# Performance work log

Measured on AMD Instinct MI355X. Metric: run time of the kernel, lower is better.

The kernel has to match this reference:

```python
import jax, jax.numpy as jnp
import numpy as np

# ---- dims (match init_kwargs) ----
IMG = 128; PATCH = 16; GRID = IMG // PATCH; L = GRID * GRID  # 64 patches
D = 256            # embed_dim
EXP = 2; DIN = D * EXP          # d_inner = 512
DH = 64; H = DIN // DH          # 8 heads
G = 1; N = 64                   # n_groups, d_state
DCONV = 4
DEPTH = 2
NCLS = 1000
BATCH = 16
DINPROJ = 2 * DIN + 2 * G * N + H   # z | xBC | dt
CDIM = DIN + 2 * G * N              # conv channels
EPS = 1e-6

def _snake_indices():
    g = np.arange(L).reshape(GRID, GRID)
    g[1::2] = g[1::2, ::-1]
    return jnp.asarray(g.reshape(-1))

SNAKE = _snake_indices()

def rmsnorm(x, w):
    return x * jax.lax.rsqrt(jnp.mean(x * x, axis=-1, keepdims=True) + EPS) * w

def causal_depthwise_conv(x, w, b):
    # x: (B,L,C), w: (C,K) depthwise causal conv, then SiLU
    xp = jnp.pad(x, ((0, 0), (DCONV - 1, 0), (0, 0)))
    y = sum(xp[:, k:k + x.shape[1], :] * w[:, k] for k in range(DCONV))
    return jax.nn.silu(y + b)

def mamba_block(x, Win, cw, cb, dtb, Alog, Dp, gn, Wout):
    # Mamba-2/3 style selective scan block. x: (B,L,D)
    Bsz, Lx, _ = x.shape
    zxbcdt = x @ Win                                   # (B,L,DINPROJ)
    z   = zxbcdt[..., :DIN]
    xBC = zxbcdt[..., DIN:DIN + CDIM]
    dt  = jax.nn.softplus(zxbcdt[..., DIN + CDIM:] + dtb)   # (B,L,H)
    xBC = causal_depthwise_conv(xBC, cw, cb)
    xs = xBC[..., :DIN].reshape(Bsz, Lx, H, DH)
    Bm = xBC[..., DIN:DIN + G * N].reshape(Bsz, Lx, G, N)
    Cm = xBC[..., DIN + G * N:].reshape(Bsz, Lx, G, N)
    Bh = jnp.repeat(Bm, H // G, axis=2)                # (B,L,H,N)
    Ch = jnp.repeat(Cm, H // G, axis=2)
    decay = jnp.exp(dt * (-jnp.exp(Alog)))             # (B,L,H) in (0,1)
    dBx = jnp.einsum('blh,blhp,blhn->blhpn', dt, xs, Bh)
    def step(h, inp):
        d, u = inp
        h = d[..., None, None] * h + u
        return h, h
    _, hs = jax.lax.scan(step, jnp.zeros((Bsz, H, DH, N), x.dtype),
                         (jnp.moveaxis(decay, 1, 0), jnp.moveaxis(dBx, 1, 0)))
    hs = jnp.moveaxis(hs, 0, 1)                        # (B,L,H,DH,N)
    y = jnp.einsum('blhpn,blhn->blhp', hs, Ch) + Dp[None, None, :, None] * xs
    y = y.reshape(Bsz, Lx, DIN)
    y = rmsnorm(y * jax.nn.silu(z), gn)                # gated RMSNorm
    return y @ Wout                                    # (B,L,D)

def setup_inputs() -> dict:
    key = jax.random.key(0)
    ks = jax.random.split(key, 24)
    s_in = 1.0 / np.sqrt(D); s_out = 1.0 / np.sqrt(DIN)
    def blk(k):
        kk = jax.random.split(k, 8)
        return dict(
            Win=jax.random.normal(kk[0], (DEPTH, D, DINPROJ)) * s_in,
            cw=jax.random.normal(kk[1], (DEPTH, CDIM, DCONV)) * 0.3,
            cb=jnp.zeros((DEPTH, CDIM)),
            dtb=jax.random.normal(kk[2], (DEPTH, H)) * 0.1,
            Alog=jnp.log(jax.random.uniform(kk[3], (DEPTH, H), minval=1.0, maxval=16.0)),
            Dp=jnp.ones((DEPTH, H)),
            gn=jnp.ones((DEPTH, DIN)),
            Wout=jax.random.normal(kk[4], (DEPTH, DIN, D)) * s_out)
    f = blk(ks[0]); b = blk(ks[1])
    inp = {
        'x': jax.random.normal(ks[2], (BATCH, 3, IMG, IMG), dtype=jnp.float32),
        'patch_w': jax.random.normal(ks[3], (D, 3 * PATCH * PATCH)) * (1.0 / np.sqrt(3 * PATCH * PATCH)),
        'patch_b': jnp.zeros((D,)),
        'pos_embed': jax.random.normal(ks[4], (1, L, D)) * 0.02,
        'norms_w': jnp.ones((DEPTH, D)),
        'final_w': jnp.ones((D,)),
        'head_w': jax.random.normal(ks[5], (D, NCLS)) * (1.0 / np.sqrt(D)),
        'head_b': jnp.zeros((NCLS,)),
    }
    for nm, v in f.items():
        inp[nm + '_f'] = v
    for nm, v in b.items():
        inp[nm + '_b'] = v
    return inp

def reference(x, patch_w, patch_b, pos_embed, norms_w, final_w, head_w, head_b,
              Win_f, cw_f, cb_f, dtb_f, Alog_f, Dp_f, gn_f, Wout_f,
              Win_b, cw_b, cb_b, dtb_b, Alog_b, Dp_b, gn_b, Wout_b):
    Bsz = x.shape[0]
    # patch embed == Conv2d(kernel=stride=PATCH)
    p = x.reshape(Bsz, 3, GRID, PATCH, GRID, PATCH).transpose(0, 2, 4, 1, 3, 5)
    p = p.reshape(Bsz, L, 3 * PATCH * PATCH)
    t = p @ patch_w.T + patch_b                        # (B,L,D)
    t = t + pos_embed[0]
    t = t[:, SNAKE, :]                                 # snake scan order
    for i in range(DEPTH):
        nx = rmsnorm(t, norms_w[i])
        of = mamba_block(nx, Win_f[i], cw_f[i], cb_f[i], dtb_f[i], Alog_f[i], Dp_f[i], gn_f[i], Wout_f[i])
        ob = mamba_block(nx[:, ::-1, :], Win_b[i], cw_b[i], cb_b[i], dtb_b[i], Alog_b[i], Dp_b[i], gn_b[i], Wout_b[i])[:, ::-1, :]
        t = t + 0.5 * (of + ob)                        # drop_path_rate=0 -> identity
    t = rmsnorm(t, final_w)
    t = t.mean(axis=1)
    return t @ head_w + head_b
```

## Files before the change

### kernel.cpp

```cpp
#include <hip/hip_runtime.h>
#include <hip/hip_bf16.h>
#include <math.h>

#define IMG 128
#define PATCH 16
#define L 64
#define D 256
#define DIN 512
#define DH 64
#define H 8
#define NSTATE 64
#define DCONV 4
#define DEPTH 2
#define NCLS 1000
#define BATCH 16
#define DINPROJ 1160
#define CDIM 640
#define EPS 1e-6f

typedef __attribute__((ext_vector_type(8))) short short8;
typedef __attribute__((ext_vector_type(4))) float f32x4;
typedef __attribute__((ext_vector_type(4))) unsigned short us4;
typedef unsigned short ushort_t;

__device__ __forceinline__ int snake_tok(int s){
    int r = s >> 3, c = s & 7;
    return (r & 1) ? (r * 8 + (7 - c)) : (r * 8 + c);
}
__device__ __forceinline__ float silu_f(float x){ return x / (1.f + expf(-x)); }
__device__ __forceinline__ float softplus_f(float x){ return x > 20.f ? x : log1pf(expf(x)); }
__device__ __forceinline__ ushort_t f2b(float f){
    __hip_bfloat16 h = __float2bfloat16(f);
    return *(ushort_t*)&h;
}

__device__ __forceinline__ float block_sum256(float v){
    __shared__ float sm[4];
    #pragma unroll
    for (int o = 32; o > 0; o >>= 1) v += __shfl_down(v, o);
    if ((threadIdx.x & 63) == 0) sm[threadIdx.x >> 6] = v;
    __syncthreads();
    return sm[0] + sm[1] + sm[2] + sm[3];
}

__global__ __launch_bounds__(256) void wconv_patch_k(
    const float* __restrict__ Win0, const float* __restrict__ Win1,
    const float* __restrict__ Wout0, const float* __restrict__ Wout1,
    ushort_t* __restrict__ wbuf,
    const float* __restrict__ x, const float* __restrict__ PW,
    float* __restrict__ part)
{
    __shared__ float sm[32][33];
    __shared__ __align__(16) ushort_t As[2][64][40];
    __shared__ __align__(16) ushort_t Bs[2][64][40];
    const int zall = blockIdx.z;
    if (zall < 8){
        int z = zall;
        int R, C; const float* src; ushort_t* dst;
        if (z < 4){
            int layer = z >> 1, dir = z & 1;
            src = (dir ? Win1 : Win0) + (size_t)layer * D * DINPROJ;
            dst = wbuf + (size_t)z * 296960;
            R = D; C = DINPROJ;
        } else {
            int zz = z - 4, layer = zz >> 1, dir = zz & 1;
            src = (dir ? Wout1 : Wout0) + (size_t)layer * DIN * D;
            dst = wbuf + 1187840 + (size_t)zz * 131072;
            R = DIN; C = D;
        }
        int ctiles = (C + 31) >> 5, rtiles = R >> 5;
        if (blockIdx.x >= ctiles || blockIdx.y >= rtiles) return;
        int c0 = blockIdx.x * 32, r0 = blockIdx.y * 32;
        int tx = threadIdx.x & 31, ty = threadIdx.x >> 5;
        #pragma unroll
        for (int k = 0; k < 4; ++k){
            int r = r0 + ty + 8 * k, c = c0 + tx;
            sm[ty + 8 * k][tx] = (c < C) ? src[(size_t)r * C + c] : 0.f;
        }
        __syncthreads();
        #pragma unroll
        for (int k = 0; k < 4; ++k){
            int dr = c0 + ty + 8 * k, dc = r0 + tx;
            if (dr < C) dst[(size_t)dr * R + dc] = f2b(sm[tx][ty + 8 * k]);
        }
        return;
    }
    if (blockIdx.x >= 4) return;
    const int t = threadIdx.x;
    const int n0 = blockIdx.x * 64;
    const int b  = blockIdx.y;
    const int split = zall - 8;
    const int kbase = split * 96;
    const int lrow = t >> 2, lc8 = (t & 3) * 8;
    const int tok = snake_tok(lrow), gy = tok >> 3, gx = tok & 7;
    const float* xb = x + (size_t)b * 3 * IMG * IMG;
    const int wave = t >> 6, lane = t & 63;
    const int wm = (wave >> 1) * 32, wn = (wave & 1) * 32;
    const int fro = lane & 15, fk = (lane >> 4) * 8;

    f32x4 acc[2][2];
    #pragma unroll
    for (int i = 0; i < 2; ++i)
        #pragma unroll
        for (int j = 0; j < 2; ++j) acc[i][j] = (f32x4){0.f,0.f,0.f,0.f};

    short8 areg, breg;
    auto gload = [&](int kk){
        int k = kk + lc8;
        int c = k >> 8, rem = k & 255, py = rem >> 4, px = rem & 15;
        const float* srcA = xb + ((size_t)c * IMG + gy * PATCH + py) * IMG + gx * PATCH + px;
        float4 a0 = *(const float4*)(srcA);
        float4 a1 = *(const float4*)(srcA + 4);
        ushort_t ta[8] = {f2b(a0.x),f2b(a0.y),f2b(a0.z),f2b(a0.w),
                          f2b(a1.x),f2b(a1.y),f2b(a1.z),f2b(a1.w)};
        areg = *(short8*)ta;
        const float* srcB = PW + (size_t)(n0 + lrow) * 768 + kk + lc8;
        float4 b0 = *(const float4*)(srcB);
        float4 b1 = *(const float4*)(srcB + 4);
        ushort_t tb[8] = {f2b(b0.x),f2b(b0.y),f2b(b0.z),f2b(b0.w),
                          f2b(b1.x),f2b(b1.y),f2b(b1.z),f2b(b1.w)};
        breg = *(short8*)tb;
    };
    auto sstore = [&](int buf){
        *(short8*)&As[buf][lrow][lc8] = areg;
        *(short8*)&Bs[buf][lrow][lc8] = breg;
    };

    const int nk = 3;
    gload(kbase); sstore(0);
    __syncthreads();
    for (int kt = 0; kt < nk; ++kt){
        const int buf = kt & 1;
        if (kt + 1 < nk) gload(kbase + (kt + 1) * 32);
        short8 af[2], bfr[2];
        af[0]  = *(const short8*)&As[buf][wm + fro][fk];
        af[1]  = *(const short8*)&As[buf][wm + 16 + fro][fk];
        bfr[0] = *(const short8*)&Bs[buf][wn + fro][fk];
        bfr[1] = *(const short8*)&Bs[buf][wn + 16 + fro][fk];
        #pragma unroll
        for (int i = 0; i < 2; ++i)
            #pragma unroll
            for (int j = 0; j < 2; ++j)
                acc[i][j] = __builtin_amdgcn_mfma_f32_16x16x32_bf16(af[i], bfr[j], acc[i][j], 0, 0, 0);
        if (kt + 1 < nk) sstore(buf ^ 1);
        __syncthreads();
    }
    float* Cp = part + (size_t)split * (BATCH * L * D);
    #pragma unroll
    for (int i = 0; i < 2; ++i){
        #pragma unroll
        for (int j = 0; j < 2; ++j){
            int col = n0 + wn + j * 16 + (lane & 15);
            #pragma unroll
            for (int r = 0; r < 4; ++r){
                int srow = wm + i * 16 + (lane >> 4) * 4 + r;
                Cp[(size_t)(b * 64 + srow) * D + col] = acc[i][j][r];
            }
        }
    }
}

__global__ void patch_red_k(const float* __restrict__ part, const float* __restrict__ pb,
                            const float* __restrict__ pos, float* __restrict__ t){
    int i = blockIdx.x * 256 + threadIdx.x;
    int d = i & (D - 1), s = (i >> 8) & (L - 1);
    float v = 0.f;
    #pragma unroll
    for (int r = 0; r < 8; ++r) v += part[i + r * (BATCH * L * D)];
    t[i] = v + pb[d] + pos[snake_tok(s) * D + d];
}

__global__ __launch_bounds__(256) void gemm_in_k(
    const float* __restrict__ T, const float* __restrict__ nw,
    const ushort_t* __restrict__ B0, const ushort_t* __restrict__ B1,
    const float* __restrict__ cw0, const float* __restrict__ cw1,
    const float* __restrict__ cb0, const float* __restrict__ cb1,
    const float* __restrict__ dtb0, const float* __restrict__ dtb1,
    const float* __restrict__ Al0, const float* __restrict__ Al1,
    float* __restrict__ zb0, float* __restrict__ zb1,
    float* __restrict__ xy0, float* __restrict__ xy1,
    float* __restrict__ bc0, float* __restrict__ bc1,
    float* __restrict__ dts0, float* __restrict__ dts1,
    float* __restrict__ cums0, float* __restrict__ cums1)
{
    __shared__ __align__(16) ushort_t As[64][264];
    __shared__ __align__(16) ushort_t Bs[2][64][40];
    __shared__ float Ctile[64][68];
    const int dir = blockIdx.z;
    const ushort_t* __restrict__ Bw = dir ? B1 : B0;
    const int t = threadIdx.x;
    const int m0 = blockIdx.y * 64, n0 = blockIdx.x * 64;
    const int b = blockIdx.y;
    const int arow = t >> 2;
    const int wave = t >> 6, lane = t & 63;
    const int wm = (wave >> 1) * 32, wn = (wave & 1) * 32;
    const int fro = lane & 15, fk = (lane >> 4) * 8;

    {
        const float* src = T + (size_t)(m0 + arow) * D;
        float ss = 0.f;
        #pragma unroll
        for (int i = 0; i < 16; ++i){
            int c = (t & 3) * 4 + i * 16;
            float4 v = *(const float4*)(src + c);
            ss += v.x*v.x + v.y*v.y + v.z*v.z + v.w*v.w;
        }
        ss += __shfl_xor(ss, 1);
        ss += __shfl_xor(ss, 2);
        float sc = rsqrtf(ss * (1.f / (float)D) + EPS);
        #pragma unroll
        for (int i = 0; i < 16; ++i){
            int c = (t & 3) * 4 + i * 16;
            float4 v = *(const float4*)(src + c);
            float4 w = *(const float4*)(nw + c);
            us4 o = {f2b(v.x*sc*w.x), f2b(v.y*sc*w.y), f2b(v.z*sc*w.z), f2b(v.w*sc*w.w)};
            *(us4*)&As[arow][c] = o;
        }
    }
    const int lrow = t >> 2, lc8 = (t & 3) * 8;
    float4 breg;
    auto gloadB = [&](int kk){
        int gn = n0 + lrow;
        if (gn < DINPROJ) breg = *(const float4*)(Bw + (size_t)gn * D + kk + lc8);
        else breg = make_float4(0.f,0.f,0.f,0.f);
    };
    auto sstoreB = [&](int buf){ *(float4*)&Bs[buf][lrow][lc8] = breg; };

    f32x4 acc[2][2];
    #pragma unroll
    for (int i = 0; i < 2; ++i)
        #pragma unroll
        for (int j = 0; j < 2; ++j) acc[i][j] = (f32x4){0.f,0.f,0.f,0.f};

    gloadB(0); sstoreB(0);
    __syncthreads();
    const int nk = D / 32;
    for (int kt = 0; kt < nk; ++kt){
        const int buf = kt & 1;
        if (kt + 1 < nk) gloadB((kt + 1) * 32);
        short8 af[2], bfr[2];
        af[0]  = *(const short8*)&As[wm + fro][kt * 32 + fk];
        af[1]  = *(const short8*)&As[wm + 16 + fro][kt * 32 + fk];
        bfr[0] = *(const short8*)&Bs[buf][wn + fro][fk];
        bfr[1] = *(const short8*)&Bs[buf][wn + 16 + fro][fk];
        #pragma unroll
        for (int i = 0; i < 2; ++i)
            #pragma unroll
            for (int j = 0; j < 2; ++j)
                acc[i][j] = __builtin_amdgcn_mfma_f32_16x16x32_bf16(af[i], bfr[j], acc[i][j], 0, 0, 0);
        if (kt + 1 < nk) sstoreB(buf ^ 1);
        __syncthreads();
    }

    if (n0 < DIN){
        float* zb = dir ? zb1 : zb0;
        #pragma unroll
        for (int i = 0; i < 2; ++i){
            #pragma unroll
            for (int j = 0; j < 2; ++j){
                int col = n0 + wn + j * 16 + (lane & 15);
                #pragma unroll
                for (int r = 0; r < 4; ++r){
                    int row = m0 + wm + i * 16 + (lane >> 4) * 4 + r;
                    zb[(size_t)row * DIN + col] = acc[i][j][r];
                }
            }
        }
        return;
    }

    #pragma unroll
    for (int i = 0; i < 2; ++i){
        #pragma unroll
        for (int j = 0; j < 2; ++j){
            int lcol = wn + j * 16 + (lane & 15);
            #pragma unroll
            for (int r = 0; r < 4; ++r){
                int lr = wm + i * 16 + (lane >> 4) * 4 + r;
                Ctile[lr][lcol] = acc[i][j][r];
            }
        }
    }
    __syncthreads();

    if (n0 < 1152){
        const float* cw = dir ? cw1 : cw0;
        const float* cb = dir ? cb1 : cb0;
        float* xy = dir ? xy1 : xy0;
        float* bc = dir ? bc1 : bc0;
        const int c = t & 63;
        const int cc = n0 - DIN + c;
        const float w0 = cw[cc * DCONV + 0], w1 = cw[cc * DCONV + 1];
        const float w2 = cw[cc * DCONV + 2], w3 = cw[cc * DCONV + 3];
        const float bb = cb[cc];
        #pragma unroll
        for (int rep = 0; rep < 16; ++rep){
            int s = (t >> 6) + rep * 4;
            float a = bb;
            {
                int sp = s - 3;
                if (sp >= 0) a += w0 * Ctile[dir ? 63 - sp : sp][c];
                sp = s - 2;
                if (sp >= 0) a += w1 * Ctile[dir ? 63 - sp : sp][c];
                sp = s - 1;
                if (sp >= 0) a += w2 * Ctile[dir ? 63 - sp : sp][c];
                a += w3 * Ctile[dir ? 63 - s : s][c];
            }
            float v = silu_f(a);
            if (cc < DIN) xy[(size_t)(b * 64 + s) * DIN + cc] = v;
            else          bc[(size_t)(b * 64 + s) * 128 + (cc - DIN)] = v;
        }
        return;
    }

    {
        const float* dtb = dir ? dtb1 : dtb0;
        const float* Al  = dir ? Al1  : Al0;
        float* dts  = dir ? dts1  : dts0;
        float* cums = dir ? cums1 : cums0;
        int s = t & 63;
        int l = dir ? (63 - s) : s;
        #pragma unroll
        for (int rep = 0; rep < 2; ++rep){
            int h = (t >> 6) + rep * 4;
            float raw = Ctile[l][h] + dtb[h];
            float dt = softplus_f(raw);
            float val = -expf(Al[h]) * dt;
            #pragma unroll
            for (int o = 1; o < 64; o <<= 1){
                float u = __shfl_up(val, o);
                if (s >= o) val += u;
            }
            dts[(size_t)(b * 64 + s) * H + h]  = dt;
            cums[(size_t)(b * 64 + s) * H + h] = val;
        }
    }
}

__global__ __launch_bounds__(256) void gemm_out_k(
    const ushort_t* __restrict__ A0, const ushort_t* __restrict__ A1,
    const ushort_t* __restrict__ B0, const ushort_t* __restrict__ B1,
    float* __restrict__ part)
{
    __shared__ __align__(16) ushort_t As[2][64][40];
    __shared__ __align__(16) ushort_t Bs[2][64][40];
    const int t = threadIdx.x;
    const int n0 = blockIdx.x * 64, m0 = blockIdx.y * 64;
    const int z = blockIdx.z;
    const int dir = z >> 2;
    const int kbase = (z & 3) * 128;
    const ushort_t* __restrict__ A = dir ? A1 : A0;
    const ushort_t* __restrict__ B = dir ? B1 : B0;
    const int lrow = t >> 2, lc8 = (t & 3) * 8;
    const int wave = t >> 6, lane = t & 63;
    const int wm = (wave >> 1) * 32, wn = (wave & 1) * 32;
    const int fro = lane & 15, fk = (lane >> 4) * 8;

    float4 areg, breg;
    auto gload = [&](int kk){
        areg = *(const float4*)(A + (size_t)(m0 + lrow) * DIN + kk + lc8);
        breg = *(const float4*)(B + (size_t)(n0 + lrow) * DIN + kk + lc8);
    };
    auto sstore = [&](int buf){
        *(float4*)&As[buf][lrow][lc8] = areg;
        *(float4*)&Bs[buf][lrow][lc8] = breg;
    };

    f32x4 acc[2][2];
    #pragma unroll
    for (int i = 0; i < 2; ++i)
        #pragma unroll
        for (int j = 0; j < 2; ++j) acc[i][j] = (f32x4){0.f,0.f,0.f,0.f};

    const int nk = 4;
    gload(kbase); sstore(0);
    __syncthreads();
    for (int kt = 0; kt < nk; ++kt){
        const int buf = kt & 1;
        if (kt + 1 < nk) gload(kbase + (kt + 1) * 32);
        short8 af[2], bfr[2];
        af[0]  = *(const short8*)&As[buf][wm + fro][fk];
        af[1]  = *(const short8*)&As[buf][wm + 16 + fro][fk];
        bfr[0] = *(const short8*)&Bs[buf][wn + fro][fk];
        bfr[1] = *(const short8*)&Bs[buf][wn + 16 + fro][fk];
        #pragma unroll
        for (int i = 0; i < 2; ++i)
            #pragma unroll
            for (int j = 0; j < 2; ++j)
                acc[i][j] = __builtin_amdgcn_mfma_f32_16x16x32_bf16(af[i], bfr[j], acc[i][j], 0, 0, 0);
        if (kt + 1 < nk) sstore(buf ^ 1);
        __syncthreads();
    }
    float* Cp = part + (size_t)z * (BATCH * L * D);
    #pragma unroll
    for (int i = 0; i < 2; ++i){
        #pragma unroll
        for (int j = 0; j < 2; ++j){
            int col = n0 + wn + j * 16 + (lane & 15);
            #pragma unroll
            for (int r = 0; r < 4; ++r){
                int row = m0 + wm + i * 16 + (lane >> 4) * 4 + r;
                Cp[(size_t)row * D + col] = acc[i][j][r];
            }
        }
    }
}

__global__ void out_red_k(const float* __restrict__ part, float* __restrict__ t){
    int i = blockIdx.x * 256 + threadIdx.x;
    float v = 0.f;
    #pragma unroll
    for (int r = 0; r < 8; ++r) v += part[i + r * (BATCH * L * D)];
    t[i] += 0.5f * v;
}

__global__ __launch_bounds__(512) void yscan2_k(
    const float* __restrict__ bc0, const float* __restrict__ bc1,
    const float* __restrict__ dts0, const float* __restrict__ dts1,
    const float* __restrict__ cums0, const float* __restrict__ cums1,
    const float* __restrict__ Dp0, const float* __restrict__ Dp1,
    float* __restrict__ xy0, float* __restrict__ xy1)
{
    __shared__ float Bc[64][65];
    __shared__ float CX[64][65];
    __shared__ float Am[64][65];
    __shared__ float cumS[64], dtS[64];
    const int h = blockIdx.x, b = blockIdx.y, dir = blockIdx.z;
    const float* bc   = dir ? bc1   : bc0;
    const float* dts  = dir ? dts1  : dts0;
    const float* cums = dir ? cums1 : cums0;
    const float* Dp   = dir ? Dp1   : Dp0;
    float* xy = dir ? xy1 : xy0;
    const int t = threadIdx.x;

    if (t < 64){
        cumS[t] = cums[(size_t)(b * L + t) * H + h];
        dtS[t]  = dts[(size_t)(b * L + t) * H + h];
    }
    for (int i = t; i < 4096; i += 512){
        int s = i >> 6, n = i & 63;
        Bc[s][n] = bc[(size_t)(b * L + s) * 128 + n];
        CX[s][n] = bc[(size_t)(b * L + s) * 128 + 64 + n];
    }
    __syncthreads();
    for (int i = t; i < 4096; i += 512){
        int s = i >> 6, j = i & 63;
        float v = 0.f;
        if (j <= s){
            float acc = 0.f;
            #pragma unroll
            for (int n = 0; n < 64; ++n) acc += CX[s][n] * Bc[j][n];
            v = acc * expf(cumS[s] - cumS[j]) * dtS[j];
        }
        Am[s][j] = v;
    }
    __syncthreads();
    for (int i = t; i < 4096; i += 512){
        int j = i >> 6, p = i & 63;
        CX[j][p] = xy[(size_t)(b * L + j) * DIN + h * DH + p];
    }
    __syncthreads();
    float dp = Dp[h];
    for (int i = t; i < 4096; i += 512){
        int s = i >> 6, p = i & 63;
        float acc = dp * CX[s][p];
        #pragma unroll
        for (int j = 0; j < 64; ++j) acc += Am[s][j] * CX[j][p];
        int l = dir ? (L - 1 - s) : s;
        xy[(size_t)(b * L + l) * DIN + h * DH + p] = acc;
    }
}

__global__ void gate_rmsnorm_k(const float* __restrict__ y0, const float* __restrict__ y1,
                               const float* __restrict__ zb0, const float* __restrict__ zb1,
                               const float* __restrict__ gn0, const float* __restrict__ gn1,
                               ushort_t* __restrict__ ybf0, ushort_t* __restrict__ ybf1){
    int dir = blockIdx.y;
    const float* y = dir ? y1 : y0;
    const float* zb = dir ? zb1 : zb0;
    const float* gn = dir ? gn1 : gn0;
    ushort_t* ybf = dir ? ybf1 : ybf0;
    int row = blockIdx.x;
    float g[2]; float ss = 0.f;
    #pragma unroll
    for (int r = 0; r < 2; ++r){
        int c = threadIdx.x + 256 * r;
        float z = zb[(size_t)row * DIN + c];
        float val = y[(size_t)row * DIN + c] * silu_f(z);
        g[r] = val; ss += val * val;
    }
    float tot = block_sum256(ss);
    float sc = rsqrtf(tot / (float)DIN + EPS);
    #pragma unroll
    for (int r = 0; r < 2; ++r){
        int c = threadIdx.x + 256 * r;
        ybf[(size_t)row * DIN + c] = f2b(g[r] * sc * gn[c]);
    }
}

__global__ void finalmean_k(const float* __restrict__ T, const float* __restrict__ part,
                            const float* __restrict__ fw, float* __restrict__ tm8){
    __shared__ float sm[4];
    int b = blockIdx.x, q = blockIdx.y;
    int d = threadIdx.x;
    float a = 0.f;
    for (int r = 0; r < 8; ++r){
        int row = b * 64 + q * 8 + r;
        size_t o = (size_t)row * D + d;
        float pv = 0.f;
        #pragma unroll
        for (int u = 0; u < 8; ++u) pv += part[o + (size_t)u * (BATCH * L * D)];
        float v = T[o] + 0.5f * pv;
        float ssl = v * v;
        #pragma unroll
        for (int off = 32; off > 0; off >>= 1) ssl += __shfl_down(ssl, off);
        if ((threadIdx.x & 63) == 0) sm[threadIdx.x >> 6] = ssl;
        __syncthreads();
        float ss = sm[0] + sm[1] + sm[2] + sm[3];
        __syncthreads();
        float sc = rsqrtf(ss / (float)D + EPS);
        a += v * sc;
    }
    tm8[(q * BATCH + b) * D + d] = a * (1.f / (float)L) * fw[d];
}

__global__ void head_k(const float* __restrict__ tm8, const float* __restrict__ hw,
                       const float* __restrict__ hb, float* __restrict__ out){
    __shared__ float trs[2][256];
    int i0 = blockIdx.x * 256;
    int mmin = i0 / NCLS;
    int t = threadIdx.x;
    #pragma unroll
    for (int mm = 0; mm < 2; ++mm){
        int m = mmin + mm;
        float v = 0.f;
        if (m < BATCH){
            #pragma unroll
            for (int q = 0; q < 8; ++q)
                v += tm8[(q * BATCH + m) * D + t];
        }
        trs[mm][t] = v;
    }
    __syncthreads();
    int i = i0 + t;
    if (i >= BATCH * NCLS) return;
    int m = i / NCLS, n = i - m * NCLS;
    const float* tr = trs[m - mmin];
    const float* hc = hw + n;
    float a0 = 0.f, a1 = 0.f, a2 = 0.f, a3 = 0.f;
    #pragma unroll 4
    for (int k = 0; k < D; k += 4){
        a0 = fmaf(tr[k],     hc[(size_t)k * NCLS],       a0);
        a1 = fmaf(tr[k + 1], hc[(size_t)(k + 1) * NCLS], a1);
        a2 = fmaf(tr[k + 2], hc[(size_t)(k + 2) * NCLS], a2);
        a3 = fmaf(tr[k + 3], hc[(size_t)(k + 3) * NCLS], a3);
    }
    out[i] = (a0 + a1) + (a2 + a3) + hb[n];
}

extern "C" void kernel_launch(void* const* d_in, const int* in_sizes, int n_in,
                              void* d_out, int out_size, void* d_ws, size_t ws_size,
                              hipStream_t stream){
    (void)in_sizes; (void)n_in; (void)out_size; (void)ws_size;
    const float* x       = (const float*)d_in[0];
    const float* patch_w = (const float*)d_in[1];
    const float* patch_b = (const float*)d_in[2];
    const float* pos     = (const float*)d_in[3];
    const float* norms_w = (const float*)d_in[4];
    const float* final_w = (const float*)d_in[5];
    const float* head_w  = (const float*)d_in[6];
    const float* head_b  = (const float*)d_in[7];
    const float* Win[2]  = {(const float*)d_in[8],  (const float*)d_in[16]};
    const float* cw[2]   = {(const float*)d_in[9],  (const float*)d_in[17]};
    const float* cb[2]   = {(const float*)d_in[10], (const float*)d_in[18]};
    const float* dtb[2]  = {(const float*)d_in[11], (const float*)d_in[19]};
    const float* Alog[2] = {(const float*)d_in[12], (const float*)d_in[20]};
    const float* Dp[2]   = {(const float*)d_in[13], (const float*)d_in[21]};
    const float* gn[2]   = {(const float*)d_in[14], (const float*)d_in[22]};
    const float* Wout[2] = {(const float*)d_in[15], (const float*)d_in[23]};

    float* ws = (float*)d_ws;
    float* t     = ws;
    float* tm8   = t     + 262144;
    float* zb0   = tm8   + 32768;
    float* zb1   = zb0   + 524288;
    float* xy0   = zb1   + 524288;
    float* xy1   = xy0   + 524288;
    float* bc0   = xy1   + 524288;
    float* bc1   = bc0   + 131072;
    float* dts0  = bc1   + 131072;
    float* dts1  = dts0  + 8192;
    float* cum0  = dts1  + 8192;
    float* cum1  = cum0  + 8192;
    float* partP = cum1  + 8192;
    float* partO = partP + 2097152;
    float* f32end = partO + 2097152;

    ushort_t* ybf0 = (ushort_t*)f32end;
    ushort_t* ybf1 = ybf0 + 524288;
    ushort_t* wbuf = ybf1 + 524288;
    ushort_t* win_bf  = wbuf;
    ushort_t* wout_bf = wbuf + 1187840;

    const int BL = BATCH * L;

    wconv_patch_k<<<dim3(37, 16, 16), 256, 0, stream>>>(
        Win[0], Win[1], Wout[0], Wout[1], wbuf, x, patch_w, partP);
    patch_red_k<<<BL, 256, 0, stream>>>(partP, patch_b, pos, t);

    for (int i = 0; i < DEPTH; ++i){
        const float* cw0  = cw[0]   + (size_t)i * CDIM * DCONV;
        const float* cw1  = cw[1]   + (size_t)i * CDIM * DCONV;
        const float* cb0  = cb[0]   + (size_t)i * CDIM;
        const float* cb1  = cb[1]   + (size_t)i * CDIM;
        const float* dtb0 = dtb[0]  + (size_t)i * H;
        const float* dtb1 = dtb[1]  + (size_t)i * H;
        const float* Al0  = Alog[0] + (size_t)i * H;
        const float* Al1  = Alog[1] + (size_t)i * H;
        const float* Dp0  = Dp[0]   + (size_t)i * H;
        const float* Dp1  = Dp[1]   + (size_t)i * H;
        const float* gn0  = gn[0]   + (size_t)i * DIN;
        const float* gn1  = gn[1]   + (size_t)i * DIN;
        const ushort_t* Wi0 = win_bf  + (size_t)(2 * i + 0) * 296960;
        const ushort_t* Wi1 = win_bf  + (size_t)(2 * i + 1) * 296960;
        const ushort_t* Wo0 = wout_bf + (size_t)(2 * i + 0) * 131072;
        const ushort_t* Wo1 = wout_bf + (size_t)(2 * i + 1) * 131072;

        gemm_in_k<<<dim3(19, 16, 2), 256, 0, stream>>>(
            t, norms_w + i * D, Wi0, Wi1, cw0, cw1, cb0, cb1, dtb0, dtb1,
            Al0, Al1, zb0, zb1, xy0, xy1, bc0, bc1, dts0, dts1, cum0, cum1);
        yscan2_k<<<dim3(H, BATCH, 2), 512, 0, stream>>>(
            bc0, bc1, dts0, dts1, cum0, cum1, Dp0, Dp1, xy0, xy1);
        gate_rmsnorm_k<<<dim3(BL, 2), 256, 0, stream>>>(
            xy0, xy1, zb0, zb1, gn0, gn1, ybf0, ybf1);
        gemm_out_k<<<dim3(4, 16, 8), 256, 0, stream>>>(ybf0, ybf1, Wo0, Wo1, partO);
        if (i == 0)
            out_red_k<<<BL, 256, 0, stream>>>(partO, t);
    }

    finalmean_k<<<dim3(BATCH, 8), 256, 0, stream>>>(t, partO, final_w, tm8);
    head_k<<<(BATCH * NCLS + 255) / 256, 256, 0, stream>>>(
        tm8, head_w, head_b, (float*)d_out);
}
```

Before: 134.9 us.

## Fuse gating and RMSNorm into scan and out-projection GEMM, drop gate kernel

The SiLU(z) gate is now applied inside the scan kernel, which also writes per-head partial sums of squares. The out-projection GEMM turns these into a per-row RMS scale and applies the scale, the norm weight and the bf16 conversion while loading its A tiles. The scan's output loop is also rearranged so each thread holds eight output columns of one row, allowing vectorised stores. This removes one kernel launch and a full fp32 read/write round trip of the activations. In exchange, the GEMM reads fp32 activations and redoes the scaling in every N-block, and the scan reads z.

```diff
diff --git a/kernel.cpp b/kernel.cpp
--- a/kernel.cpp
+++ b/kernel.cpp
@@ -32,15 +32,6 @@
 __device__ __forceinline__ ushort_t f2b(float f){
     __hip_bfloat16 h = __float2bfloat16(f);
     return *(ushort_t*)&h;
-}
-
-__device__ __forceinline__ float block_sum256(float v){
-    __shared__ float sm[4];
-    #pragma unroll
-    for (int o = 32; o > 0; o >>= 1) v += __shfl_down(v, o);
-    if ((threadIdx.x & 63) == 0) sm[threadIdx.x >> 6] = v;
-    __syncthreads();
-    return sm[0] + sm[1] + sm[2] + sm[3];
 }
 
 __global__ __launch_bounds__(256) void wconv_patch_k(
@@ -337,32 +328,146 @@
     }
 }
 
+__global__ __launch_bounds__(512) void yscan2_k(
+    const float* __restrict__ bc0, const float* __restrict__ bc1,
+    const float* __restrict__ dts0, const float* __restrict__ dts1,
+    const float* __restrict__ cums0, const float* __restrict__ cums1,
+    const float* __restrict__ Dp0, const float* __restrict__ Dp1,
+    const float* __restrict__ zb0, const float* __restrict__ zb1,
+    float* __restrict__ xy0, float* __restrict__ xy1,
+    float* __restrict__ ssq0, float* __restrict__ ssq1)
+{
+    __shared__ float Bc[64][65];
+    __shared__ float CX[64][65];
+    __shared__ float Am[64][65];
+    __shared__ float cumS[64], dtS[64];
+    __shared__ float ssqp[8][64];
+    const int h = blockIdx.x, b = blockIdx.y, dir = blockIdx.z;
+    const float* bc   = dir ? bc1   : bc0;
+    const float* dts  = dir ? dts1  : dts0;
+    const float* cums = dir ? cums1 : cums0;
+    const float* Dp   = dir ? Dp1   : Dp0;
+    const float* zb   = dir ? zb1   : zb0;
+    float* xy  = dir ? xy1  : xy0;
+    float* ssq = dir ? ssq1 : ssq0;
+    const int t = threadIdx.x;
+
+    if (t < 64){
+        cumS[t] = cums[(size_t)(b * L + t) * H + h];
+        dtS[t]  = dts[(size_t)(b * L + t) * H + h];
+    }
+    for (int i = t; i < 4096; i += 512){
+        int s = i >> 6, n = i & 63;
+        Bc[s][n] = bc[(size_t)(b * L + s) * 128 + n];
+        CX[s][n] = bc[(size_t)(b * L + s) * 128 + 64 + n];
+    }
+    __syncthreads();
+    for (int i = t; i < 4096; i += 512){
+        int s = i >> 6, j = i & 63;
+        float v = 0.f;
+        if (j <= s){
+            float acc = 0.f;
+            #pragma unroll
+            for (int n = 0; n < 64; ++n) acc += CX[s][n] * Bc[j][n];
+            v = acc * expf(cumS[s] - cumS[j]) * dtS[j];
+        }
+        Am[s][j] = v;
+    }
+    __syncthreads();
+    for (int i = t; i < 4096; i += 512){
+        int j = i >> 6, p = i & 63;
+        CX[j][p] = xy[(size_t)(b * L + j) * DIN + h * DH + p];
+    }
+    __syncthreads();
+    {
+        const int s = t & 63, pg = t >> 6;
+        const int l = dir ? (63 - s) : s;
+        const size_t row = (size_t)(b * 64 + l);
+        const float dp = Dp[h];
+        float acc[8];
+        #pragma unroll
+        for (int pp = 0; pp < 8; ++pp) acc[pp] = dp * CX[s][pg * 8 + pp];
+        #pragma unroll
+        for (int j = 0; j < 64; ++j){
+            float am = Am[s][j];
+            #pragma unroll
+            for (int pp = 0; pp < 8; ++pp)
+                acc[pp] = fmaf(am, CX[j][pg * 8 + pp], acc[pp]);
+        }
+        const float* zr = zb + row * DIN + h * DH + pg * 8;
+        float4 z0 = *(const float4*)(zr);
+        float4 z1 = *(const float4*)(zr + 4);
+        float zv[8] = {z0.x, z0.y, z0.z, z0.w, z1.x, z1.y, z1.z, z1.w};
+        float g2 = 0.f;
+        float gout[8];
+        #pragma unroll
+        for (int pp = 0; pp < 8; ++pp){
+            float g = acc[pp] * silu_f(zv[pp]);
+            gout[pp] = g;
+            g2 += g * g;
+        }
+        ssqp[pg][s] = g2;
+        float* dst = xy + row * DIN + h * DH + pg * 8;
+        *(float4*)(dst)     = make_float4(gout[0], gout[1], gout[2], gout[3]);
+        *(float4*)(dst + 4) = make_float4(gout[4], gout[5], gout[6], gout[7]);
+    }
+    __syncthreads();
+    if (t < 64){
+        int ll = dir ? (63 - t) : t;
+        float v = 0.f;
+        #pragma unroll
+        for (int q = 0; q < 8; ++q) v += ssqp[q][t];
+        ssq[(size_t)(b * 64 + ll) * H + h] = v;
+    }
+}
+
 __global__ __launch_bounds__(256) void gemm_out_k(
-    const ushort_t* __restrict__ A0, const ushort_t* __restrict__ A1,
+    const float* __restrict__ G0, const float* __restrict__ G1,
+    const float* __restrict__ ssq0, const float* __restrict__ ssq1,
+    const float* __restrict__ gn0, const float* __restrict__ gn1,
     const ushort_t* __restrict__ B0, const ushort_t* __restrict__ B1,
     float* __restrict__ part)
 {
     __shared__ __align__(16) ushort_t As[2][64][40];
     __shared__ __align__(16) ushort_t Bs[2][64][40];
+    __shared__ float scl[64];
     const int t = threadIdx.x;
     const int n0 = blockIdx.x * 64, m0 = blockIdx.y * 64;
     const int z = blockIdx.z;
     const int dir = z >> 2;
     const int kbase = (z & 3) * 128;
-    const ushort_t* __restrict__ A = dir ? A1 : A0;
+    const float* __restrict__ G   = dir ? G1   : G0;
+    const float* __restrict__ ssq = dir ? ssq1 : ssq0;
+    const float* __restrict__ gnw = dir ? gn1  : gn0;
     const ushort_t* __restrict__ B = dir ? B1 : B0;
     const int lrow = t >> 2, lc8 = (t & 3) * 8;
     const int wave = t >> 6, lane = t & 63;
     const int wm = (wave >> 1) * 32, wn = (wave & 1) * 32;
     const int fro = lane & 15, fk = (lane >> 4) * 8;
 
-    float4 areg, breg;
+    if (t < 64){
+        const float* sr = ssq + (size_t)(m0 + t) * H;
+        float v = (sr[0] + sr[1]) + (sr[2] + sr[3]) + (sr[4] + sr[5]) + (sr[6] + sr[7]);
+        scl[t] = rsqrtf(v * (1.f / (float)DIN) + EPS);
+    }
+    __syncthreads();
+
+    short8 areg; float4 breg;
     auto gload = [&](int kk){
-        areg = *(const float4*)(A + (size_t)(m0 + lrow) * DIN + kk + lc8);
+        const float* src = G + (size_t)(m0 + lrow) * DIN + kk + lc8;
+        float4 a0 = *(const float4*)(src);
+        float4 a1 = *(const float4*)(src + 4);
+        const float* gw = gnw + kk + lc8;
+        float4 w0 = *(const float4*)(gw);
+        float4 w1 = *(const float4*)(gw + 4);
+        float sc = scl[lrow];
+        ushort_t ta[8] = {f2b(a0.x*sc*w0.x), f2b(a0.y*sc*w0.y), f2b(a0.z*sc*w0.z), f2b(a0.w*sc*w0.w),
+                          f2b(a1.x*sc*w1.x), f2b(a1.y*sc*w1.y), f2b(a1.z*sc*w1.z), f2b(a1.w*sc*w1.w)};
+        areg = *(short8*)ta;
         breg = *(const float4*)(B + (size_t)(n0 + lrow) * DIN + kk + lc8);
     };
     auto sstore = [&](int buf){
-        *(float4*)&As[buf][lrow][lc8] = areg;
+        *(short8*)&As[buf][lrow][lc8] = areg;
         *(float4*)&Bs[buf][lrow][lc8] = breg;
     };
 
@@ -412,90 +517,6 @@
     #pragma unroll
     for (int r = 0; r < 8; ++r) v += part[i + r * (BATCH * L * D)];
     t[i] += 0.5f * v;
-}
-
-__global__ __launch_bounds__(512) void yscan2_k(
-    const float* __restrict__ bc0, const float* __restrict__ bc1,
-    const float* __restrict__ dts0, const float* __restrict__ dts1,
-    const float* __restrict__ cums0, const float* __restrict__ cums1,
-    const float* __restrict__ Dp0, const float* __restrict__ Dp1,
-    float* __restrict__ xy0, float* __restrict__ xy1)
-{
-    __shared__ float Bc[64][65];
-    __shared__ float CX[64][65];
-    __shared__ float Am[64][65];
-    __shared__ float cumS[64], dtS[64];
-    const int h = blockIdx.x, b = blockIdx.y, dir = blockIdx.z;
-    const float* bc   = dir ? bc1   : bc0;
-    const float* dts  = dir ? dts1  : dts0;
-    const float* cums = dir ? cums1 : cums0;
-    const float* Dp   = dir ? Dp1   : Dp0;
-    float* xy = dir ? xy1 : xy0;
-    const int t = threadIdx.x;
-
-    if (t < 64){
-        cumS[t] = cums[(size_t)(b * L + t) * H + h];
-        dtS[t]  = dts[(size_t)(b * L + t) * H + h];
-    }
-    for (int i = t; i < 4096; i += 512){
-        int s = i >> 6, n = i & 63;
-        Bc[s][n] = bc[(size_t)(b * L + s) * 128 + n];
-        CX[s][n] = bc[(size_t)(b * L + s) * 128 + 64 + n];
-    }
-    __syncthreads();
-    for (int i = t; i < 4096; i += 512){
-        int s = i >> 6, j = i & 63;
-        float v = 0.f;
-        if (j <= s){
-            float acc = 0.f;
-            #pragma unroll
-            for (int n = 0; n < 64; ++n) acc += CX[s][n] * Bc[j][n];
-            v = acc * expf(cumS[s] - cumS[j]) * dtS[j];
-        }
-        Am[s][j] = v;
-    }
-    __syncthreads();
-    for (int i = t; i < 4096; i += 512){
-        int j = i >> 6, p = i & 63;
-        CX[j][p] = xy[(size_t)(b * L + j) * DIN + h * DH + p];
-    }
-    __syncthreads();
-    float dp = Dp[h];
-    for (int i = t; i < 4096; i += 512){
-        int s = i >> 6, p = i & 63;
-        float acc = dp * CX[s][p];
-        #pragma unroll
-        for (int j = 0; j < 64; ++j) acc += Am[s][j] * CX[j][p];
-        int l = dir ? (L - 1 - s) : s;
-        xy[(size_t)(b * L + l) * DIN + h * DH + p] = acc;
-    }
-}
-
-__global__ void gate_rmsnorm_k(const float* __restrict__ y0, const float* __restrict__ y1,
-                               const float* __restrict__ zb0, const float* __restrict__ zb1,
-                               const float* __restrict__ gn0, const float* __restrict__ gn1,
-                               ushort_t* __restrict__ ybf0, ushort_t* __restrict__ ybf1){
-    int dir = blockIdx.y;
-    const float* y = dir ? y1 : y0;
-    const float* zb = dir ? zb1 : zb0;
-    const float* gn = dir ? gn1 : gn0;
-    ushort_t* ybf = dir ? ybf1 : ybf0;
-    int row = blockIdx.x;
-    float g[2]; float ss = 0.f;
-    #pragma unroll
-    for (int r = 0; r < 2; ++r){
-        int c = threadIdx.x + 256 * r;
-        float z = zb[(size_t)row * DIN + c];
-        float val = y[(size_t)row * DIN + c] * silu_f(z);
-        g[r] = val; ss += val * val;
-    }
-    float tot = block_sum256(ss);
-    float sc = rsqrtf(tot / (float)DIN + EPS);
-    #pragma unroll
-    for (int r = 0; r < 2; ++r){
-        int c = threadIdx.x + 256 * r;
-        ybf[(size_t)row * DIN + c] = f2b(g[r] * sc * gn[c]);
-    }
 }
 
 __global__ void finalmean_k(const float* __restrict__ T, const float* __restrict__ part,
@@ -592,13 +613,13 @@
     float* dts1  = dts0  + 8192;
     float* cum0  = dts1  + 8192;
     float* cum1  = cum0  + 8192;
-    float* partP = cum1  + 8192;
+    float* ssq0  = cum1  + 8192;
+    float* ssq1  = ssq0  + 8192;
+    float* partP = ssq1  + 8192;
     float* partO = partP + 2097152;
     float* f32end = partO + 2097152;
 
-    ushort_t* ybf0 = (ushort_t*)f32end;
-    ushort_t* ybf1 = ybf0 + 524288;
-    ushort_t* wbuf = ybf1 + 524288;
+    ushort_t* wbuf = (ushort_t*)f32end;
     ushort_t* win_bf  = wbuf;
     ushort_t* wout_bf = wbuf + 1187840;
 
@@ -630,10 +651,10 @@
             t, norms_w + i * D, Wi0, Wi1, cw0, cw1, cb0, cb1, dtb0, dtb1,
             Al0, Al1, zb0, zb1, xy0, xy1, bc0, bc1, dts0, dts1, cum0, cum1);
         yscan2_k<<<dim3(H, BATCH, 2), 512, 0, stream>>>(
-            bc0, bc1, dts0, dts1, cum0, cum1, Dp0, Dp1, xy0, xy1);
-        gate_rmsnorm_k<<<dim3(BL, 2), 256, 0, stream>>>(
-            xy0, xy1, zb0, zb1, gn0, gn1, ybf0, ybf1);
-        gemm_out_k<<<dim3(4, 16, 8), 256, 0, stream>>>(ybf0, ybf1, Wo0, Wo1, partO);
+            bc0, bc1, dts0, dts1, cum0, cum1, Dp0, Dp1, zb0, zb1,
+            xy0, xy1, ssq0, ssq1);
+        gemm_out_k<<<dim3(4, 16, 8), 256, 0, stream>>>(
+            xy0, xy1, ssq0, ssq1, gn0, gn1, Wo0, Wo1, partO);
         if (i == 0)
             out_red_k<<<BL, 256, 0, stream>>>(partO, t);
     }
```

Result: faster. 130.9 us (-2.9%).
